# Kernel optimization log

Hardware: AMD Instinct MI355X
Metric: run time of the kernel (lower is better)

## Reference

```python
import jax, jax.numpy as jnp
import numpy as np

D_MODEL = 1024
NUM_HEADS = 16
D_K = D_MODEL // NUM_HEADS
B, S = 4, 2048
NEG_INF = -1e9


def _linear_params(key, d_out, d_in):
    k1, k2 = jax.random.split(key)
    lim = 1.0 / np.sqrt(d_in)
    w = jax.random.uniform(k1, (d_out, d_in), jnp.float32, -lim, lim)
    b = jax.random.uniform(k2, (d_out,), jnp.float32, -lim, lim)
    return w, b


def setup_inputs() -> dict:
    key = jax.random.key(0)
    ks = jax.random.split(key, 16)
    query = jax.random.normal(ks[0], (B, S, D_MODEL), jnp.float32)
    kk = jax.random.normal(ks[1], (B, S, D_MODEL), jnp.float32)
    vv = jax.random.normal(ks[2], (B, S, D_MODEL), jnp.float32)
    # causal mask, broadcastable to [B,H,Sq,Sk]
    mask = jnp.tril(jnp.ones((S, S), jnp.int32))[None, None]
    wq1, bq1 = _linear_params(ks[3], D_MODEL, D_MODEL)
    wq2, bq2 = _linear_params(ks[4], D_MODEL, D_MODEL)
    wk1, bk1 = _linear_params(ks[5], D_MODEL, D_MODEL)
    wk2, bk2 = _linear_params(ks[6], D_MODEL, D_MODEL)
    wv1, bv1 = _linear_params(ks[7], D_MODEL, D_MODEL)
    wv2, bv2 = _linear_params(ks[8], D_MODEL, D_MODEL)
    wo, bo = _linear_params(ks[9], D_MODEL, D_MODEL)
    return dict(query=query, key=kk, value=vv, mask=mask,
                wq1=wq1, bq1=bq1, wq2=wq2, bq2=bq2,
                wk1=wk1, bk1=bk1, wk2=wk2, bk2=bk2,
                wv1=wv1, bv1=bv1, wv2=wv2, bv2=bv2,
                wo=wo, bo=bo)


def _swiglu_proj(x, w1, b1, w2, b2):
    # F.silu(w1(x)) * w2(x)
    return jax.nn.silu(x @ w1.T + b1) * (x @ w2.T + b2)


def _split_heads(x):
    b, s, _ = x.shape
    return x.reshape(b, s, NUM_HEADS, D_K).transpose(0, 2, 1, 3)  # [B,H,S,dk]


def reference(query, key, value, mask,
              wq1, bq1, wq2, bq2,
              wk1, bk1, wk2, bk2,
              wv1, bv1, wv2, bv2,
              wo, bo):
    q = _split_heads(_swiglu_proj(query, wq1, bq1, wq2, bq2))
    k = _split_heads(_swiglu_proj(key, wk1, bk1, wk2, bk2))
    v = _split_heads(_swiglu_proj(value, wv1, bv1, wv2, bv2))
    scores = jnp.einsum('bhqd,bhkd->bhqk', q, k) / np.sqrt(D_K).astype(np.float32)
    scores = jnp.where(mask == 0, jnp.float32(NEG_INF), scores)
    attn = jax.nn.softmax(scores, axis=-1)
    x = jnp.einsum('bhqk,bhkd->bhqd', attn, v)  # [B,H,S,dk]
    x = x.transpose(0, 2, 1, 3).reshape(query.shape[0], -1, NUM_HEADS * D_K)
    return x @ wo.T + bo
```

## Files before the change

kernel.cpp:

```cpp
#include <hip/hip_runtime.h>


typedef __bf16 bf16;
typedef bf16 bf16x8 __attribute__((ext_vector_type(8)));
typedef float f32x4 __attribute__((ext_vector_type(4)));
typedef unsigned short u16;
typedef unsigned int u32;
typedef u16 u16x8 __attribute__((ext_vector_type(8)));
typedef u16 u16x4 __attribute__((ext_vector_type(4)));

#define DEVI static __device__ __forceinline__

DEVI u16 f2b(float f) {
  union { float f; u32 u; } v; v.f = f;
  u32 r = v.u + 0x7FFFu + ((v.u >> 16) & 1u);
  return (u16)(r >> 16);
}
DEVI f32x4 mfma16(bf16x8 a, bf16x8 b, f32x4 c) {
  return __builtin_amdgcn_mfma_f32_16x16x32_bf16(a, b, c, 0, 0, 0);
}
DEVI void gload16(const void* g, void* l) {
  __builtin_amdgcn_global_load_lds(
      (const __attribute__((address_space(1))) void*)g,
      (__attribute__((address_space(3))) void*)l, 16, 0, 0);
}
DEVI u32 cvtpk(float lo, float hi) {
  u32 r;
  asm("v_cvt_pk_bf16_f32 %0, %1, %2" : "=v"(r) : "v"(lo), "v"(hi));
  return r;
}
DEVI void pswap(u32& a, u32& b) {
  asm("v_permlane32_swap_b32 %0, %1" : "+v"(a), "+v"(b));
}

struct P6 { const float* p[6]; };

__global__ void cvt_wpair(P6 in, u16* __restrict__ out) {
  const int pair = blockIdx.y;
  const float* w1 = in.p[2 * pair];
  const float* w2 = in.p[2 * pair + 1];
  u16* dst = out + (size_t)pair * 2097152;
  const int i = blockIdx.x * 256 + threadIdx.x;
  const int v = i >> 7;
  const int k0 = (i & 127) << 3;
  const int t7 = v & 127;
  const int g = (t7 >> 4) & 1;
  const int c = (v >> 7) * 64 + ((t7 >> 5) << 4) + (t7 & 15);
  const float* src = (g ? w2 : w1) + (size_t)c * 1024 + k0;
  const f32x4 a = *(const f32x4*)src;
  const f32x4 b = *(const f32x4*)(src + 4);
  u16x8 wv;
#pragma unroll
  for (int j = 0; j < 4; ++j) { wv[j] = f2b(a[j]); wv[4 + j] = f2b(b[j]); }
  *(u16x8*)(dst + (size_t)v * 1024 + k0) = wv;
}

__global__ void cvt_x(const float* __restrict__ s0, u16* __restrict__ d0,
                      const float* __restrict__ s1, u16* __restrict__ d1) {
  const float* src = blockIdx.y ? s1 : s0;
  u16* dst = blockIdx.y ? d1 : d0;
  const int i = blockIdx.x * 256 + threadIdx.x;
  const f32x4 a = ((const f32x4*)src)[i * 2];
  const f32x4 b = ((const f32x4*)src)[i * 2 + 1];
  u16x8 w;
#pragma unroll
  for (int j = 0; j < 4; ++j) { w[j] = f2b(a[j]); w[4 + j] = f2b(b[j]); }
  ((u16x8*)dst)[i] = w;
}

struct GArgs {
  const u16* A; const u16* W;
  const float* b1; const float* b2;
  void* out; float scale;
};

template<int MODE, bool DUAL>
__global__ __launch_bounds__(256, 2) void gemm128(GArgs g0, GArgs g1)
{
  __shared__ char smem[65536];
  const int fl = blockIdx.x;
  const GArgs g = (DUAL && fl >= 1024) ? g1 : g0;
  const int local = DUAL ? (fl & 1023) : fl;
  const int t = threadIdx.x;
  const int lane = t & 63, wid = t >> 6;
  const int lg = lane >> 4, lc = lane & 15;
  const int wr = (wid >> 1) * 64, wc = (wid & 1) * 64;
  constexpr int NXB = (MODE == 2) ? 8 : 16;
  const int xcd = local & 7, w8 = local >> 3;
  const int m0 = (xcd * 8 + w8 / NXB) * 128;
  const int bx = w8 % NXB;
  const int K = 1024;
  const int srow = lane >> 3, scolb = (lane & 7) << 4;

  const f32x4 fz = {0.f, 0.f, 0.f, 0.f};
  f32x4 acc[4][4];
#pragma unroll
  for (int i = 0; i < 4; ++i)
#pragma unroll
    for (int j = 0; j < 4; ++j) acc[i][j] = fz;

  auto STAGE = [&](int buf, int kt) {
    const int k0 = kt << 6;
    char* As = smem + buf * 32768;
    char* Ws = As + 16384;
#pragma unroll
    for (int p = 0; p < 4; ++p) {
      const int rb = wid * 32 + p * 8;
      const int row = rb + srow;
      const int ce = (scolb ^ ((row & 7) << 4)) >> 1;
      gload16(g.A + (size_t)(m0 + row) * K + k0 + ce, As + rb * 128);
      gload16(g.W + (size_t)(bx * 128 + row) * K + k0 + ce, Ws + rb * 128);
    }
  };

  STAGE(0, 0);
  __syncthreads();
  for (int kt = 0; kt < 16; ++kt) {
    const int cur = kt & 1;
    if (kt < 15) STAGE(cur ^ 1, kt + 1);
    const char* As = smem + cur * 32768;
    const char* Ws = As + 16384;
#pragma unroll
    for (int kh = 0; kh < 2; ++kh) {
      bf16x8 af[4], bfr[4];
#pragma unroll
      for (int mf = 0; mf < 4; ++mf) {
        const int r = wr + mf * 16 + lc;
        af[mf] = *(const bf16x8*)(As + r * 128 + ((kh * 64 + (lg << 4)) ^ ((r & 7) << 4)));
      }
#pragma unroll
      for (int nf = 0; nf < 4; ++nf) {
        const int v = wc + nf * 16 + lc;
        bfr[nf] = *(const bf16x8*)(Ws + v * 128 + ((kh * 64 + (lg << 4)) ^ ((v & 7) << 4)));
      }
#pragma unroll
      for (int mf = 0; mf < 4; ++mf)
#pragma unroll
        for (int nf = 0; nf < 4; ++nf)
          acc[mf][nf] = mfma16(af[mf], bfr[nf], acc[mf][nf]);
    }
    __syncthreads();
  }
  if constexpr (MODE == 2) {
    float* Co = (float*)g.out;
#pragma unroll
    for (int mf = 0; mf < 4; ++mf)
#pragma unroll
      for (int nf = 0; nf < 4; ++nf) {
        const int r0 = m0 + wr + mf * 16 + (lg << 2);
        const int C = bx * 128 + wc + nf * 16 + lc;
        const float bv = g.b1[C];
#pragma unroll
        for (int j = 0; j < 4; ++j)
          Co[(size_t)(r0 + j) * 1024 + C] = acc[mf][nf][j] + bv;
      }
  } else {
    u16* Co = (u16*)g.out;
#pragma unroll
    for (int mf = 0; mf < 4; ++mf) {
      const int r0 = m0 + wr + mf * 16 + (lg << 2);
#pragma unroll
      for (int p = 0; p < 2; ++p) {
        const int C = bx * 64 + (wid & 1) * 32 + p * 16 + lc;
        const float b1v = g.b1[C], b2v = g.b2[C];
        const int h = C >> 6, d = C & 63;
        if constexpr (MODE == 0) {
#pragma unroll
          for (int j = 0; j < 4; ++j) {
            const int r = r0 + j;
            const float x = acc[mf][2 * p][j] + b1v;
            const float y = acc[mf][2 * p + 1][j] + b2v;
            const float vv = (x / (1.f + __expf(-x))) * y * g.scale;
            const int bb = r >> 11, s = r & 2047;
            Co[((size_t)(bb * 16 + h) * 2048 + s) * 64 + d] = f2b(vv);
          }
        } else {
          u16x4 wv;
#pragma unroll
          for (int j = 0; j < 4; ++j) {
            const float x = acc[mf][2 * p][j] + b1v;
            const float y = acc[mf][2 * p + 1][j] + b2v;
            wv[j] = f2b((x / (1.f + __expf(-x))) * y);
          }
          const int bb = r0 >> 11, s0 = r0 & 2047;
          *(u16x4*)(Co + ((size_t)(bb * 16 + h) * 64 + d) * 2048 + s0) = wv;
        }
      }
    }
  }
}

__global__ __launch_bounds__(256, 4) void attn_fwd(
    const u16* __restrict__ Q, const u16* __restrict__ Kk,
    const u16* __restrict__ Vt, u16* __restrict__ O)
{
  __shared__ char smem[32768];
  const int t = threadIdx.x;
  const int lane = t & 63, wid = t >> 6;
  const int lg = lane >> 4, lc = lane & 15;
  const int flat = blockIdx.x;
  const int bh = flat & 63;
  const int qc = 15 - (flat >> 6);
  const int b = bh >> 4, h = bh & 15;
  const f32x4 fz = {0.f, 0.f, 0.f, 0.f};
  const float THR = 11.5f;
  const bool ev = ((lg & 1) == 0);

  auto STAGE = [&](int buf, int kt) {
    const int kbase = kt << 6;
    char* Kb = smem + buf * 16384;
    char* Vb = Kb + 8192;
#pragma unroll
    for (int p = 0; p < 4; ++p) {
      const int idx = wid * 4 + p;
      const int rb = (idx & 7) * 8;
      const int row = rb + (lane >> 3);
      const int ce = (((lane & 7) << 4) ^ ((row & 7) << 4)) >> 1;
      if (idx < 8)
        gload16(Kk + ((size_t)bh * 2048 + kbase + row) * 64 + ce, Kb + rb * 128);
      else
        gload16(Vt + ((size_t)bh * 64 + row) * 2048 + kbase + ce, Vb + rb * 128);
    }
  };

  const int qw = qc * 128 + wid * 32;

  bf16x8 qf[2][2];
#pragma unroll
  for (int qg = 0; qg < 2; ++qg)
#pragma unroll
    for (int kh = 0; kh < 2; ++kh)
      qf[qg][kh] = *(const bf16x8*)(Q + ((size_t)bh * 2048 + qw + qg * 16 + lc) * 64 + kh * 32 + lg * 8);

  f32x4 o[2][4];
#pragma unroll
  for (int qg = 0; qg < 2; ++qg)
#pragma unroll
    for (int dn = 0; dn < 4; ++dn) o[qg][dn] = fz;
  float mrow[2] = {-1e30f, -1e30f}, lsum[2] = {0.f, 0.f};

  const int nt = 2 * qc + 2;
  STAGE(0, 0);
  __syncthreads();
  for (int kt = 0; kt < nt; ++kt) {
    const int cur = kt & 1;
    if (kt + 1 < nt) STAGE(cur ^ 1, kt + 1);
    const int kbase = kt << 6;
    const char* Ks = smem + cur * 16384;
    const char* Vs = Ks + 8192;
    if (kbase <= qw + 31) {
      f32x4 sfT[4][2];
#pragma unroll
      for (int nf = 0; nf < 4; ++nf)
#pragma unroll
        for (int qg = 0; qg < 2; ++qg) sfT[nf][qg] = fz;
      __builtin_amdgcn_s_setprio(1);
#pragma unroll
      for (int kh = 0; kh < 2; ++kh) {
        bf16x8 kb[4];
#pragma unroll
        for (int nf = 0; nf < 4; ++nf) {
          const int r = nf * 16 + lc;
          kb[nf] = *(const bf16x8*)(Ks + r * 128 + ((kh * 64 + (lg << 4)) ^ ((r & 7) << 4)));
        }
#pragma unroll
        for (int nf = 0; nf < 4; ++nf) {
          sfT[nf][0] = mfma16(kb[nf], qf[0][kh], sfT[nf][0]);
          sfT[nf][1] = mfma16(kb[nf], qf[1][kh], sfT[nf][1]);
        }
      }
      __builtin_amdgcn_s_setprio(0);
      if (kbase + 63 > qw) {
#pragma unroll
        for (int qg = 0; qg < 2; ++qg) {
          const int qq = qw + qg * 16 + lc;
#pragma unroll
          for (int nf = 0; nf < 4; ++nf)
#pragma unroll
            for (int j = 0; j < 4; ++j)
              if (kbase + nf * 16 + (lg << 2) + j > qq) sfT[nf][qg][j] = -1e30f;
        }
      }
      float pm[2];
#pragma unroll
      for (int qg = 0; qg < 2; ++qg) {
        float m = sfT[0][qg][0];
#pragma unroll
        for (int nf = 0; nf < 4; ++nf)
#pragma unroll
          for (int j = 0; j < 4; ++j) m = fmaxf(m, sfT[nf][qg][j]);
        m = fmaxf(m, __shfl_xor(m, 16));
        m = fmaxf(m, __shfl_xor(m, 32));
        pm[qg] = m;
      }
      const bool ok = (pm[0] <= mrow[0] + THR) && (pm[1] <= mrow[1] + THR);
      if (!__all(ok)) {
#pragma unroll
        for (int qg = 0; qg < 2; ++qg) {
          const float mn = fmaxf(mrow[qg], pm[qg]);
          const float sc = exp2f(mrow[qg] - mn);
          mrow[qg] = mn;
          lsum[qg] *= sc;
#pragma unroll
          for (int dn = 0; dn < 4; ++dn)
#pragma unroll
            for (int j = 0; j < 4; ++j) o[qg][dn][j] *= sc;
        }
      }
#pragma unroll
      for (int qg = 0; qg < 2; ++qg)
#pragma unroll
        for (int nf = 0; nf < 4; ++nf)
#pragma unroll
          for (int j = 0; j < 4; ++j) {
            const float p = exp2f(sfT[nf][qg][j] - mrow[qg]);
            sfT[nf][qg][j] = p;
            lsum[qg] += p;
          }
      u32 pw[2][2][4];
#pragma unroll
      for (int qg = 0; qg < 2; ++qg)
#pragma unroll
        for (int kh = 0; kh < 2; ++kh) {
          u32 A0 = cvtpk(sfT[2 * kh][qg][0], sfT[2 * kh][qg][1]);
          u32 A1 = cvtpk(sfT[2 * kh][qg][2], sfT[2 * kh][qg][3]);
          u32 B0 = cvtpk(sfT[2 * kh + 1][qg][0], sfT[2 * kh + 1][qg][1]);
          u32 B1 = cvtpk(sfT[2 * kh + 1][qg][2], sfT[2 * kh + 1][qg][3]);
          pswap(A0, B0);
          pswap(A1, B1);
          const u32 P0s = __shfl_xor(A0, 16);
          const u32 Q0s = __shfl_xor(B0, 16);
          const u32 P1s = __shfl_xor(A1, 16);
          const u32 Q1s = __shfl_xor(B1, 16);
          pw[qg][kh][0] = ev ? A0 : Q0s;
          pw[qg][kh][1] = ev ? A1 : Q1s;
          pw[qg][kh][2] = ev ? P0s : B0;
          pw[qg][kh][3] = ev ? P1s : B1;
        }
      __builtin_amdgcn_s_setprio(1);
#pragma unroll
      for (int kh = 0; kh < 2; ++kh) {
        union { u32 u[4]; bf16x8 v; } p0, p1;
#pragma unroll
        for (int w = 0; w < 4; ++w) { p0.u[w] = pw[0][kh][w]; p1.u[w] = pw[1][kh][w]; }
#pragma unroll
        for (int dn = 0; dn < 4; ++dn) {
          const int vr = dn * 16 + lc;
          const bf16x8 vb = *(const bf16x8*)(Vs + vr * 128 + ((kh * 64 + (lg << 4)) ^ ((vr & 7) << 4)));
          o[0][dn] = mfma16(vb, p0.v, o[0][dn]);
          o[1][dn] = mfma16(vb, p1.v, o[1][dn]);
        }
      }
      __builtin_amdgcn_s_setprio(0);
    }
    __syncthreads();
  }
#pragma unroll
  for (int qg = 0; qg < 2; ++qg) {
    float l = lsum[qg];
    l += __shfl_xor(l, 16);
    l += __shfl_xor(l, 32);
    const float inv = __builtin_amdgcn_rcpf(l);
    const size_t ob = ((size_t)(b * 2048 + qw + qg * 16 + lc) * 16 + h) * 64 + (lg << 2);
#pragma unroll
    for (int dn = 0; dn < 4; ++dn) {
      u16x4 wv;
#pragma unroll
      for (int j = 0; j < 4; ++j) wv[j] = f2b(o[qg][dn][j] * inv);
      *(u16x4*)(O + ob + dn * 16) = wv;
    }
  }
}

extern "C" void kernel_launch(void* const* d_in, const int* in_sizes, int n_in,
                              void* d_out, int out_size, void* d_ws, size_t ws_size,
                              hipStream_t stream)
{
  (void)in_sizes; (void)n_in; (void)out_size; (void)ws_size;
  const float* xq  = (const float*)d_in[0];
  const float* xk  = (const float*)d_in[1];
  const float* xv  = (const float*)d_in[2];
  const float* wq1 = (const float*)d_in[4];
  const float* bq1 = (const float*)d_in[5];
  const float* wq2 = (const float*)d_in[6];
  const float* bq2 = (const float*)d_in[7];
  const float* wk1 = (const float*)d_in[8];
  const float* bk1 = (const float*)d_in[9];
  const float* wk2 = (const float*)d_in[10];
  const float* bk2 = (const float*)d_in[11];
  const float* wv1 = (const float*)d_in[12];
  const float* bv1 = (const float*)d_in[13];
  const float* wv2 = (const float*)d_in[14];
  const float* bv2 = (const float*)d_in[15];
  const float* wo  = (const float*)d_in[16];
  const float* bo  = (const float*)d_in[17];

  char* ws = (char*)d_ws;
  u16* WB = (u16*)ws;
  u16* XQ = (u16*)(ws + 14680064);
  u16* XK = (u16*)(ws + 31457280);
  u16* QB = (u16*)(ws + 48234496);
  u16* KB = (u16*)(ws + 65011712);
  u16* VT = (u16*)(ws + 81788928);
  u16* XV = XQ;
  u16* AO = XK;
  u16* WCQ = WB;
  u16* WCK = WB + 2097152;
  u16* WCV = WB + 4194304;
  u16* WO  = WB + 6291456;

  P6 p6 = {{wq1, wq2, wk1, wk2, wv1, wv2}};
  cvt_wpair<<<dim3(1024, 3), 256, 0, stream>>>(p6, WB);
  cvt_x<<<dim3(512, 1), 256, 0, stream>>>(wo, WO, wo, WO);
  cvt_x<<<dim3(4096, 2), 256, 0, stream>>>(xq, XQ, xk, XK);

  const float QSCALE = 0.125f * 1.44269504088896f;
  GArgs gq = {XQ, WCQ, bq1, bq2, QB, QSCALE};
  GArgs gk = {XK, WCK, bk1, bk2, KB, 1.0f};
  gemm128<0, true><<<2048, 256, 0, stream>>>(gq, gk);

  cvt_x<<<dim3(4096, 1), 256, 0, stream>>>(xv, XV, xv, XV);
  GArgs gv = {XV, WCV, bv1, bv2, VT, 1.0f};
  gemm128<1, false><<<1024, 256, 0, stream>>>(gv, gv);

  attn_fwd<<<1024, 256, 0, stream>>>(QB, KB, VT, AO);

  GArgs go = {AO, WO, bo, nullptr, d_out, 1.0f};
  gemm128<2, false><<<512, 256, 0, stream>>>(go, go);
}
```

Measured before the change: 237.5 us.

## Split causal attention KV range into two halves and merge with LSE

Each query chunk's causal key range is split into two halves handled by separate blocks, doubling the grid. Each block writes a partial normalized output plus a log-sum-exp, and a new merge kernel combines the two partials per row. This shortens the longest per-block key loop and improves load balance under the causal mask. In exchange it adds extra global traffic for the partials and the merge, plus one more kernel launch. Launch bounds are also raised to allow five blocks per CU.

```diff
diff --git a/kernel.cpp b/kernel.cpp
--- a/kernel.cpp
+++ b/kernel.cpp
@@ -15,6 +15,9 @@
   union { float f; u32 u; } v; v.f = f;
   u32 r = v.u + 0x7FFFu + ((v.u >> 16) & 1u);
   return (u16)(r >> 16);
+}
+DEVI float b2f(u16 b) {
+  union { u32 u; float f; } v; v.u = ((u32)b) << 16; return v.f;
 }
 DEVI f32x4 mfma16(bf16x8 a, bf16x8 b, f32x4 c) {
   return __builtin_amdgcn_mfma_f32_16x16x32_bf16(a, b, c, 0, 0, 0);
@@ -190,9 +193,10 @@
   }
 }
 
-__global__ __launch_bounds__(256, 4) void attn_fwd(
+__global__ __launch_bounds__(256, 5) void attn_fwd(
     const u16* __restrict__ Q, const u16* __restrict__ Kk,
-    const u16* __restrict__ Vt, u16* __restrict__ O)
+    const u16* __restrict__ Vt, u16* __restrict__ O0,
+    u16* __restrict__ O1, float* __restrict__ LSE)
 {
   __shared__ char smem[32768];
   const int t = threadIdx.x;
@@ -200,11 +204,15 @@
   const int lg = lane >> 4, lc = lane & 15;
   const int flat = blockIdx.x;
   const int bh = flat & 63;
-  const int qc = 15 - (flat >> 6);
+  const int half = (flat >> 6) & 1;
+  const int qc = 15 - (flat >> 7);
   const int b = bh >> 4, h = bh & 15;
   const f32x4 fz = {0.f, 0.f, 0.f, 0.f};
   const float THR = 11.5f;
   const bool ev = ((lg & 1) == 0);
+
+  u16* __restrict__ Op = half ? O1 : O0;
+  float* __restrict__ LSEh = LSE + half * 131072 + bh * 2048;
 
   auto STAGE = [&](int buf, int kt) {
     const int kbase = kt << 6;
@@ -224,6 +232,8 @@
   };
 
   const int qw = qc * 128 + wid * 32;
+  const int kt0   = half ? (qc + 1) : 0;
+  const int ktend = half ? (2 * qc + 2) : (qc + 1);
 
   bf16x8 qf[2][2];
 #pragma unroll
@@ -239,12 +249,11 @@
     for (int dn = 0; dn < 4; ++dn) o[qg][dn] = fz;
   float mrow[2] = {-1e30f, -1e30f}, lsum[2] = {0.f, 0.f};
 
-  const int nt = 2 * qc + 2;
-  STAGE(0, 0);
+  STAGE(kt0 & 1, kt0);
   __syncthreads();
-  for (int kt = 0; kt < nt; ++kt) {
+  for (int kt = kt0; kt < ktend; ++kt) {
     const int cur = kt & 1;
-    if (kt + 1 < nt) STAGE(cur ^ 1, kt + 1);
+    if (kt + 1 < ktend) STAGE(cur ^ 1, kt + 1);
     const int kbase = kt << 6;
     const char* Ks = smem + cur * 16384;
     const char* Vs = Ks + 8192;
@@ -360,16 +369,42 @@
     float l = lsum[qg];
     l += __shfl_xor(l, 16);
     l += __shfl_xor(l, 32);
-    const float inv = __builtin_amdgcn_rcpf(l);
-    const size_t ob = ((size_t)(b * 2048 + qw + qg * 16 + lc) * 16 + h) * 64 + (lg << 2);
+    const bool dead = (l == 0.f);
+    const float inv = dead ? 0.f : __builtin_amdgcn_rcpf(l);
+    const int qrow = qw + qg * 16 + lc;
+    if (lg == 0)
+      LSEh[qrow] = dead ? -1e30f : (mrow[qg] + __log2f(l));
+    const size_t ob = ((size_t)(b * 2048 + qrow) * 16 + h) * 64 + (lg << 2);
 #pragma unroll
     for (int dn = 0; dn < 4; ++dn) {
       u16x4 wv;
 #pragma unroll
       for (int j = 0; j < 4; ++j) wv[j] = f2b(o[qg][dn][j] * inv);
-      *(u16x4*)(O + ob + dn * 16) = wv;
+      *(u16x4*)(Op + ob + dn * 16) = wv;
     }
   }
+}
+
+__global__ void attn_merge(const u16* __restrict__ P0, const u16* __restrict__ P1,
+                           const float* __restrict__ LSE, u16* __restrict__ AO)
+{
+  const int e8 = blockIdx.x * 256 + threadIdx.x;
+  const int h = (e8 >> 3) & 15;
+  const int s = (e8 >> 7) & 2047;
+  const int b = e8 >> 18;
+  const int bh = b * 16 + h;
+  const float l0 = LSE[bh * 2048 + s];
+  const float l1 = LSE[131072 + bh * 2048 + s];
+  const float M = fmaxf(l0, l1);
+  const float w0 = exp2f(l0 - M), w1 = exp2f(l1 - M);
+  const float inv = __builtin_amdgcn_rcpf(w0 + w1);
+  const u16x8 a = ((const u16x8*)P0)[e8];
+  const u16x8 c = ((const u16x8*)P1)[e8];
+  u16x8 w;
+#pragma unroll
+  for (int j = 0; j < 8; ++j)
+    w[j] = f2b((w0 * b2f(a[j]) + w1 * b2f(c[j])) * inv);
+  ((u16x8*)AO)[e8] = w;
 }
 
 extern "C" void kernel_launch(void* const* d_in, const int* in_sizes, int n_in,
@@ -403,11 +438,14 @@
   u16* KB = (u16*)(ws + 65011712);
   u16* VT = (u16*)(ws + 81788928);
   u16* XV = XQ;
-  u16* AO = XK;
   u16* WCQ = WB;
   u16* WCK = WB + 2097152;
   u16* WCV = WB + 4194304;
   u16* WO  = WB + 6291456;
+  u16* OP1 = XQ;
+  u16* OP0 = XK;
+  float* LSE = (float*)ws;
+  u16* AO  = QB;
 
   P6 p6 = {{wq1, wq2, wk1, wk2, wv1, wv2}};
   cvt_wpair<<<dim3(1024, 3), 256, 0, stream>>>(p6, WB);
@@ -423,7 +461,8 @@
   GArgs gv = {XV, WCV, bv1, bv2, VT, 1.0f};
   gemm128<1, false><<<1024, 256, 0, stream>>>(gv, gv);
 
-  attn_fwd<<<1024, 256, 0, stream>>>(QB, KB, VT, AO);
+  attn_fwd<<<2048, 256, 0, stream>>>(QB, KB, VT, OP0, OP1, LSE);
+  attn_merge<<<4096, 256, 0, stream>>>(OP0, OP1, LSE, AO);
 
   GArgs go = {AO, WO, bo, nullptr, d_out, 1.0f};
   gemm128<2, false><<<512, 256, 0, stream>>>(go, go);
```

After: 335.4 us. 1.41x slower.

## Use 256x256 tiles with triple-buffered pipeline for SwiGLU projection GEMMs

Applied to the files above, without the earlier changes.

Replaces the 128x128 SwiGLU projection GEMM with a 512-thread 256x256-tile kernel that uses a K-step of 32, three LDS stages with explicit vmcnt waits and raw barriers, and raised wave priority around the MFMA block. Larger tiles raise arithmetic intensity and cut global/LDS traffic per FLOP. The deeper pipeline is meant to hide load latency. The output projection is split into its own specialized 128-tile kernel. The cost is 96KB of dynamic LDS, more accumulator registers and fewer blocks (512/256), which risks lower occupancy and tail effects.

```diff
diff --git a/kernel.cpp b/kernel.cpp
--- a/kernel.cpp
+++ b/kernel.cpp
@@ -75,20 +75,130 @@
 };
 
 template<int MODE, bool DUAL>
-__global__ __launch_bounds__(256, 2) void gemm128(GArgs g0, GArgs g1)
+__global__ __launch_bounds__(512, 2) void gemm256(GArgs g0, GArgs g1)
+{
+  extern __shared__ char smem[];
+  const int fl = blockIdx.x;
+  const GArgs g = (DUAL && fl >= 256) ? g1 : g0;
+  const int local = DUAL ? (fl & 255) : fl;
+  const int t = threadIdx.x;
+  const int lane = t & 63, wid = t >> 6;
+  const int lg = lane >> 4, lc = lane & 15;
+  const int wm = wid >> 2, wn = wid & 3;
+  const int xcd = local & 7, w8 = local >> 3;
+  const int m0 = (xcd * 4 + (w8 >> 3)) * 256;
+  const int bx = w8 & 7;
+  const int K = 1024;
+
+  const f32x4 fz = {0.f, 0.f, 0.f, 0.f};
+  f32x4 acc[8][4];
+#pragma unroll
+  for (int i = 0; i < 8; ++i)
+#pragma unroll
+    for (int j = 0; j < 4; ++j) acc[i][j] = fz;
+
+  const int rA = lane >> 2;
+  const int cc = lane & 3;
+
+  auto STAGE = [&](int slot, int kt) {
+    const int k0 = kt << 5;
+    char* As = smem + slot * 32768;
+    char* Bs = As + 16384;
+#pragma unroll
+    for (int q = 0; q < 2; ++q) {
+      const int row = q * 128 + wid * 16 + rA;
+      const int ce = ((cc ^ ((row >> 1) & 3)) << 3);
+      char* db = (char*)(size_t)((q * 128 + wid * 16) * 64);
+      gload16(g.A + (size_t)(m0 + row) * K + k0 + ce, As + (size_t)db);
+      gload16(g.W + (size_t)(bx * 256 + row) * K + k0 + ce, Bs + (size_t)db);
+    }
+  };
+
+  auto COMPUTE = [&](int slot) {
+    const char* As = smem + slot * 32768;
+    const char* Bs = As + 16384;
+    bf16x8 af[8], bfr[4];
+#pragma unroll
+    for (int mf = 0; mf < 8; ++mf) {
+      const int r = wm * 128 + mf * 16 + lc;
+      af[mf] = *(const bf16x8*)(As + r * 64 + ((lg ^ ((r >> 1) & 3)) << 4));
+    }
+#pragma unroll
+    for (int nf = 0; nf < 4; ++nf) {
+      const int r = wn * 64 + nf * 16 + lc;
+      bfr[nf] = *(const bf16x8*)(Bs + r * 64 + ((lg ^ ((r >> 1) & 3)) << 4));
+    }
+    __builtin_amdgcn_s_setprio(1);
+#pragma unroll
+    for (int mf = 0; mf < 8; ++mf)
+#pragma unroll
+      for (int nf = 0; nf < 4; ++nf)
+        acc[mf][nf] = mfma16(af[mf], bfr[nf], acc[mf][nf]);
+    __builtin_amdgcn_s_setprio(0);
+  };
+
+  STAGE(0, 0);
+  STAGE(1, 1);
+  asm volatile("s_waitcnt vmcnt(4)" ::: "memory");
+  __builtin_amdgcn_s_barrier();
+  for (int kt = 0; kt < 30; ++kt) {
+    STAGE((kt + 2) % 3, kt + 2);
+    COMPUTE(kt % 3);
+    asm volatile("s_waitcnt vmcnt(4)" ::: "memory");
+    __builtin_amdgcn_s_barrier();
+  }
+  COMPUTE(0);
+  asm volatile("s_waitcnt vmcnt(0)" ::: "memory");
+  __builtin_amdgcn_s_barrier();
+  COMPUTE(1);
+
+  u16* Co = (u16*)g.out;
+#pragma unroll
+  for (int mf = 0; mf < 8; ++mf) {
+    const int r0 = m0 + wm * 128 + mf * 16 + (lg << 2);
+#pragma unroll
+    for (int p = 0; p < 2; ++p) {
+      const int C = (bx * 2 + (wn >> 1)) * 64 + ((wn & 1) * 2 + p) * 16 + lc;
+      const float b1v = g.b1[C], b2v = g.b2[C];
+      const int h = C >> 6, d = C & 63;
+      if constexpr (MODE == 0) {
+#pragma unroll
+        for (int j = 0; j < 4; ++j) {
+          const int r = r0 + j;
+          const float x = acc[mf][2 * p][j] + b1v;
+          const float y = acc[mf][2 * p + 1][j] + b2v;
+          const float vv = (x / (1.f + __expf(-x))) * y * g.scale;
+          const int bb = r >> 11, s = r & 2047;
+          Co[((size_t)(bb * 16 + h) * 2048 + s) * 64 + d] = f2b(vv);
+        }
+      } else {
+        u16x4 wv;
+#pragma unroll
+        for (int j = 0; j < 4; ++j) {
+          const float x = acc[mf][2 * p][j] + b1v;
+          const float y = acc[mf][2 * p + 1][j] + b2v;
+          wv[j] = f2b((x / (1.f + __expf(-x))) * y);
+        }
+        const int bb = r0 >> 11, s0 = r0 & 2047;
+        *(u16x4*)(Co + ((size_t)(bb * 16 + h) * 64 + d) * 2048 + s0) = wv;
+      }
+    }
+  }
+}
+
+__global__ __launch_bounds__(256, 2) void gemm128o(
+    const u16* __restrict__ Ap, const u16* __restrict__ Wp,
+    const float* __restrict__ bias, float* __restrict__ Cp)
 {
   __shared__ char smem[65536];
-  const int fl = blockIdx.x;
-  const GArgs g = (DUAL && fl >= 1024) ? g1 : g0;
-  const int local = DUAL ? (fl & 1023) : fl;
+  const int local = blockIdx.x;
   const int t = threadIdx.x;
   const int lane = t & 63, wid = t >> 6;
   const int lg = lane >> 4, lc = lane & 15;
   const int wr = (wid >> 1) * 64, wc = (wid & 1) * 64;
-  constexpr int NXB = (MODE == 2) ? 8 : 16;
   const int xcd = local & 7, w8 = local >> 3;
-  const int m0 = (xcd * 8 + w8 / NXB) * 128;
-  const int bx = w8 % NXB;
+  const int m0 = (xcd * 8 + (w8 >> 3)) * 128;
+  const int bx = w8 & 7;
   const int K = 1024;
   const int srow = lane >> 3, scolb = (lane & 7) << 4;
 
@@ -108,8 +218,8 @@
       const int rb = wid * 32 + p * 8;
       const int row = rb + srow;
       const int ce = (scolb ^ ((row & 7) << 4)) >> 1;
-      gload16(g.A + (size_t)(m0 + row) * K + k0 + ce, As + rb * 128);
-      gload16(g.W + (size_t)(bx * 128 + row) * K + k0 + ce, Ws + rb * 128);
+      gload16(Ap + (size_t)(m0 + row) * K + k0 + ce, As + rb * 128);
+      gload16(Wp + (size_t)(bx * 128 + row) * K + k0 + ce, Ws + rb * 128);
     }
   };
 
@@ -141,53 +251,17 @@
     }
     __syncthreads();
   }
-  if constexpr (MODE == 2) {
-    float* Co = (float*)g.out;
-#pragma unroll
-    for (int mf = 0; mf < 4; ++mf)
-#pragma unroll
-      for (int nf = 0; nf < 4; ++nf) {
-        const int r0 = m0 + wr + mf * 16 + (lg << 2);
-        const int C = bx * 128 + wc + nf * 16 + lc;
-        const float bv = g.b1[C];
-#pragma unroll
-        for (int j = 0; j < 4; ++j)
-          Co[(size_t)(r0 + j) * 1024 + C] = acc[mf][nf][j] + bv;
-      }
-  } else {
-    u16* Co = (u16*)g.out;
-#pragma unroll
-    for (int mf = 0; mf < 4; ++mf) {
+#pragma unroll
+  for (int mf = 0; mf < 4; ++mf)
+#pragma unroll
+    for (int nf = 0; nf < 4; ++nf) {
       const int r0 = m0 + wr + mf * 16 + (lg << 2);
-#pragma unroll
-      for (int p = 0; p < 2; ++p) {
-        const int C = bx * 64 + (wid & 1) * 32 + p * 16 + lc;
-        const float b1v = g.b1[C], b2v = g.b2[C];
-        const int h = C >> 6, d = C & 63;
-        if constexpr (MODE == 0) {
-#pragma unroll
-          for (int j = 0; j < 4; ++j) {
-            const int r = r0 + j;
-            const float x = acc[mf][2 * p][j] + b1v;
-            const float y = acc[mf][2 * p + 1][j] + b2v;
-            const float vv = (x / (1.f + __expf(-x))) * y * g.scale;
-            const int bb = r >> 11, s = r & 2047;
-            Co[((size_t)(bb * 16 + h) * 2048 + s) * 64 + d] = f2b(vv);
-          }
-        } else {
-          u16x4 wv;
-#pragma unroll
-          for (int j = 0; j < 4; ++j) {
-            const float x = acc[mf][2 * p][j] + b1v;
-            const float y = acc[mf][2 * p + 1][j] + b2v;
-            wv[j] = f2b((x / (1.f + __expf(-x))) * y);
-          }
-          const int bb = r0 >> 11, s0 = r0 & 2047;
-          *(u16x4*)(Co + ((size_t)(bb * 16 + h) * 64 + d) * 2048 + s0) = wv;
-        }
-      }
-    }
-  }
+      const int C = bx * 128 + wc + nf * 16 + lc;
+      const float bv = bias[C];
+#pragma unroll
+      for (int j = 0; j < 4; ++j)
+        Cp[(size_t)(r0 + j) * 1024 + C] = acc[mf][nf][j] + bv;
+    }
 }
 
 __global__ __launch_bounds__(256, 4) void attn_fwd(
@@ -417,14 +491,13 @@
   const float QSCALE = 0.125f * 1.44269504088896f;
   GArgs gq = {XQ, WCQ, bq1, bq2, QB, QSCALE};
   GArgs gk = {XK, WCK, bk1, bk2, KB, 1.0f};
-  gemm128<0, true><<<2048, 256, 0, stream>>>(gq, gk);
+  gemm256<0, true><<<512, 512, 98304, stream>>>(gq, gk);
 
   cvt_x<<<dim3(4096, 1), 256, 0, stream>>>(xv, XV, xv, XV);
   GArgs gv = {XV, WCV, bv1, bv2, VT, 1.0f};
-  gemm128<1, false><<<1024, 256, 0, stream>>>(gv, gv);
+  gemm256<1, false><<<256, 512, 98304, stream>>>(gv, gv);
 
   attn_fwd<<<1024, 256, 0, stream>>>(QB, KB, VT, AO);
 
-  GArgs go = {AO, WO, bo, nullptr, d_out, 1.0f};
-  gemm128<2, false><<<512, 256, 0, stream>>>(go, go);
-}
+  gemm128o<<<512, 256, 0, stream>>>(AO, WO, bo, (float*)d_out);
+}
```

New measurement: 234.2 us. No clear change (-1.4%).

## Triple-buffer GEMM main loop with K=32 tiles and explicit vmcnt waits

Applied to the files above, without the earlier changes.

Replaces the double-buffered K=64 GEMM loop with a three-slot ring of K=32 tiles, issuing loads two stages ahead. Each step ends with an explicit partial wait on outstanding vector memory plus a raw barrier instead of __syncthreads. It also switches to a smaller 64-byte-row XOR swizzle and raises wave priority around the MFMA block. The goal is to hide global-to-LDS latency while cutting LDS from 64KB to 48KB. The cost is twice as many barriers per K, and the hand-counted vmcnt values must exactly match the loads in flight.

```diff
diff --git a/kernel.cpp b/kernel.cpp
--- a/kernel.cpp
+++ b/kernel.cpp
@@ -75,9 +75,9 @@
 };
 
 template<int MODE, bool DUAL>
-__global__ __launch_bounds__(256, 2) void gemm128(GArgs g0, GArgs g1)
+__global__ __launch_bounds__(256, 2) void gemmP(GArgs g0, GArgs g1)
 {
-  __shared__ char smem[65536];
+  __shared__ char smem[49152];
   const int fl = blockIdx.x;
   const GArgs g = (DUAL && fl >= 1024) ? g1 : g0;
   const int local = DUAL ? (fl & 1023) : fl;
@@ -90,7 +90,8 @@
   const int m0 = (xcd * 8 + w8 / NXB) * 128;
   const int bx = w8 % NXB;
   const int K = 1024;
-  const int srow = lane >> 3, scolb = (lane & 7) << 4;
+  const int sr16 = lane >> 2;
+  const int sc = lane & 3;
 
   const f32x4 fz = {0.f, 0.f, 0.f, 0.f};
   f32x4 acc[4][4];
@@ -99,48 +100,58 @@
 #pragma unroll
     for (int j = 0; j < 4; ++j) acc[i][j] = fz;
 
-  auto STAGE = [&](int buf, int kt) {
-    const int k0 = kt << 6;
-    char* As = smem + buf * 32768;
-    char* Ws = As + 16384;
-#pragma unroll
-    for (int p = 0; p < 4; ++p) {
-      const int rb = wid * 32 + p * 8;
-      const int row = rb + srow;
-      const int ce = (scolb ^ ((row & 7) << 4)) >> 1;
-      gload16(g.A + (size_t)(m0 + row) * K + k0 + ce, As + rb * 128);
-      gload16(g.W + (size_t)(bx * 128 + row) * K + k0 + ce, Ws + rb * 128);
+  auto STAGE = [&](int slot, int kt) {
+    const int k0 = kt << 5;
+    char* As = smem + slot * 16384;
+    char* Bs = As + 8192;
+#pragma unroll
+    for (int p = 0; p < 2; ++p) {
+      const int rb = (wid * 2 + p) * 16;
+      const int row = rb + sr16;
+      const int ce = (sc ^ ((row >> 1) & 3)) << 3;
+      gload16(g.A + (size_t)(m0 + row) * K + k0 + ce, As + rb * 64);
+      gload16(g.W + (size_t)(bx * 128 + row) * K + k0 + ce, Bs + rb * 64);
     }
   };
 
+  auto COMPUTE = [&](int slot) {
+    const char* As = smem + slot * 16384;
+    const char* Bs = As + 8192;
+    bf16x8 af[4], bfr[4];
+#pragma unroll
+    for (int mf = 0; mf < 4; ++mf) {
+      const int r = wr + mf * 16 + lc;
+      af[mf] = *(const bf16x8*)(As + r * 64 + ((lg ^ ((r >> 1) & 3)) << 4));
+    }
+#pragma unroll
+    for (int nf = 0; nf < 4; ++nf) {
+      const int r = wc + nf * 16 + lc;
+      bfr[nf] = *(const bf16x8*)(Bs + r * 64 + ((lg ^ ((r >> 1) & 3)) << 4));
+    }
+    __builtin_amdgcn_s_setprio(1);
+#pragma unroll
+    for (int mf = 0; mf < 4; ++mf)
+#pragma unroll
+      for (int nf = 0; nf < 4; ++nf)
+        acc[mf][nf] = mfma16(af[mf], bfr[nf], acc[mf][nf]);
+    __builtin_amdgcn_s_setprio(0);
+  };
+
   STAGE(0, 0);
-  __syncthreads();
-  for (int kt = 0; kt < 16; ++kt) {
-    const int cur = kt & 1;
-    if (kt < 15) STAGE(cur ^ 1, kt + 1);
-    const char* As = smem + cur * 32768;
-    const char* Ws = As + 16384;
-#pragma unroll
-    for (int kh = 0; kh < 2; ++kh) {
-      bf16x8 af[4], bfr[4];
-#pragma unroll
-      for (int mf = 0; mf < 4; ++mf) {
-        const int r = wr + mf * 16 + lc;
-        af[mf] = *(const bf16x8*)(As + r * 128 + ((kh * 64 + (lg << 4)) ^ ((r & 7) << 4)));
-      }
-#pragma unroll
-      for (int nf = 0; nf < 4; ++nf) {
-        const int v = wc + nf * 16 + lc;
-        bfr[nf] = *(const bf16x8*)(Ws + v * 128 + ((kh * 64 + (lg << 4)) ^ ((v & 7) << 4)));
-      }
-#pragma unroll
-      for (int mf = 0; mf < 4; ++mf)
-#pragma unroll
-        for (int nf = 0; nf < 4; ++nf)
-          acc[mf][nf] = mfma16(af[mf], bfr[nf], acc[mf][nf]);
-    }
-    __syncthreads();
+  STAGE(1, 1);
+  asm volatile("s_waitcnt vmcnt(4)" ::: "memory");
+  __builtin_amdgcn_s_barrier();
+  for (int kt = 0; kt < 30; ++kt) {
+    STAGE((kt + 2) % 3, kt + 2);
+    COMPUTE(kt % 3);
+    asm volatile("s_waitcnt vmcnt(4)" ::: "memory");
+    __builtin_amdgcn_s_barrier();
   }
+  COMPUTE(0);
+  asm volatile("s_waitcnt vmcnt(0)" ::: "memory");
+  __builtin_amdgcn_s_barrier();
+  COMPUTE(1);
+
   if constexpr (MODE == 2) {
     float* Co = (float*)g.out;
 #pragma unroll
@@ -417,14 +428,14 @@
   const float QSCALE = 0.125f * 1.44269504088896f;
   GArgs gq = {XQ, WCQ, bq1, bq2, QB, QSCALE};
   GArgs gk = {XK, WCK, bk1, bk2, KB, 1.0f};
-  gemm128<0, true><<<2048, 256, 0, stream>>>(gq, gk);
+  gemmP<0, true><<<2048, 256, 0, stream>>>(gq, gk);
 
   cvt_x<<<dim3(4096, 1), 256, 0, stream>>>(xv, XV, xv, XV);
   GArgs gv = {XV, WCV, bv1, bv2, VT, 1.0f};
-  gemm128<1, false><<<1024, 256, 0, stream>>>(gv, gv);
+  gemmP<1, false><<<1024, 256, 0, stream>>>(gv, gv);
 
   attn_fwd<<<1024, 256, 0, stream>>>(QB, KB, VT, AO);
 
   GArgs go = {AO, WO, bo, nullptr, d_out, 1.0f};
-  gemm128<2, false><<<512, 256, 0, stream>>>(go, go);
-}
+  gemmP<2, false><<<512, 256, 0, stream>>>(go, go);
+}
```

After: 259.0 us. 1.09x slower.
